# Optimization experiments

Hardware: AMD Instinct MI355X
Metric: run time of the kernel (lower is better)

## Reference

```python
import jax, jax.numpy as jnp
import numpy as np

R = 8
EPS = 1e-08
EPSS = 1e-12


def _diff_x(x, r):
    left = x[:, :, r:2 * r + 1]
    middle = x[:, :, 2 * r + 1:] - x[:, :, :-2 * r - 1]
    right = x[:, :, -1:] - x[:, :, -2 * r - 1:-r - 1]
    return jnp.concatenate([left, middle, right], axis=2)


def _diff_y(x, r):
    left = x[:, :, :, r:2 * r + 1]
    middle = x[:, :, :, 2 * r + 1:] - x[:, :, :, :-2 * r - 1]
    right = x[:, :, :, -1:] - x[:, :, :, -2 * r - 1:-r - 1]
    return jnp.concatenate([left, middle, right], axis=3)


def box_filter(x, r):
    # cumsum-based (2r+1)x(2r+1) box sum with clamped borders (matches torch BoxFilter)
    return _diff_y(jnp.cumsum(_diff_x(jnp.cumsum(x, axis=2), r), axis=3), r)


def bilinear_resize(x, H, W):
    # F.interpolate(mode='bilinear', align_corners=True) for NCHW
    n, c, h, w = x.shape
    ys = jnp.linspace(0.0, h - 1.0, H)
    xs = jnp.linspace(0.0, w - 1.0, W)
    y0 = jnp.floor(ys).astype(jnp.int32)
    x0 = jnp.floor(xs).astype(jnp.int32)
    y1 = jnp.minimum(y0 + 1, h - 1)
    x1 = jnp.minimum(x0 + 1, w - 1)
    wy = (ys - y0).astype(x.dtype)[None, None, :, None]
    wx = (xs - x0).astype(x.dtype)[None, None, None, :]
    rows = jnp.take(x, y0, axis=2) * (1.0 - wy) + jnp.take(x, y1, axis=2) * wy
    return jnp.take(rows, x0, axis=3) * (1.0 - wx) + jnp.take(rows, x1, axis=3) * wx


def setup_inputs() -> dict:
    key = jax.random.key(0)
    k1, k2, k3, k4 = jax.random.split(key, 4)
    return {
        "lr_x": jax.random.normal(k1, (4, 3, 256, 256), dtype=jnp.float32),
        "lr_y": jax.random.normal(k2, (4, 3, 256, 256), dtype=jnp.float32),
        "hr_x": jax.random.normal(k3, (4, 3, 1024, 1024), dtype=jnp.float32),
        "l_a": jax.random.uniform(k4, (4, 3, 256, 256), dtype=jnp.float32),
    }


def reference(lr_x, lr_y, hr_x, l_a):
    n, c, h, w = lr_x.shape
    _, _, hh, wh = hr_x.shape
    dt = lr_x.dtype

    N = box_filter(jnp.ones((1, 1, h, w), dtype=dt), R)  # local window counts

    l_a = jnp.abs(l_a) + EPSS
    l_t = l_a / jnp.sum(l_a)

    mean_a = box_filter(l_a) if False else box_filter(l_a, R) / N
    mean_a2xy = box_filter(l_a * l_a * lr_x * lr_y, R) / N
    mean_tax = box_filter(l_t * l_a * lr_x, R) / N
    mean_ay = box_filter(l_a * lr_y, R) / N
    mean_a2x2 = box_filter(l_a * l_a * lr_x * lr_x, R) / N
    mean_ax = box_filter(l_a * lr_x, R) / N

    temp = jnp.abs(mean_a2x2 - N * mean_tax * mean_ax)
    A = (mean_a2xy - N * mean_tax * mean_ay) / (temp + EPS)
    b = (mean_ay - A * mean_ax) / mean_a

    A = box_filter(A, R) / N
    b = box_filter(b, R) / N

    mean_A = bilinear_resize(A, hh, wh)
    mean_b = bilinear_resize(b, hh, wh)
    return (mean_A * hr_x + mean_b).astype(jnp.float32)
```

## Files before the change

### kernel.cpp

```cpp
#include <hip/hip_runtime.h>

#define RAD 8
#define HH 256
#define WW 256
#define NC 12
#define PS (HH*WW)
#define SCALE (255.0f/1023.0f)

#define NA2 36
#define NC2 20
#define AP2 37
#define HP2 21

__device__ __forceinline__ int swz3072(int b) { return (b & 7) * 384 + (b >> 3); }

__device__ __forceinline__ float run17(float x) {
    float s = x + __shfl_up(x, 1, 64);
    s += __shfl_up(s, 2, 64);
    s += __shfl_up(s, 4, 64);
    s += __shfl_up(s, 8, 64);
    s += __shfl_up(x, 16, 64);
    return s;
}

__global__ __launch_bounds__(256) void k_reduce(const float* __restrict__ la,
                                                float* __restrict__ partials) {
    int tid = threadIdx.x;
    __shared__ float ls[4];
    const float4* p4 = (const float4*)la;
    int base = blockIdx.x * 2048 + tid;
    float s = 0.f;
    #pragma unroll
    for (int i = 0; i < 8; i++) {
        float4 v = p4[base + i * 256];
        s += (fabsf(v.x) + 1e-12f) + (fabsf(v.y) + 1e-12f) +
             (fabsf(v.z) + 1e-12f) + (fabsf(v.w) + 1e-12f);
    }
    for (int off = 32; off > 0; off >>= 1) s += __shfl_down(s, off, 64);
    int lane = tid & 63, wid = tid >> 6;
    if (lane == 0) ls[wid] = s;
    __syncthreads();
    if (tid == 0) partials[blockIdx.x] = ls[0] + ls[1] + ls[2] + ls[3];
}

__global__ __launch_bounds__(256) void k_tile(const float* __restrict__ la,
                                              const float* __restrict__ lx,
                                              const float* __restrict__ ly,
                                              const float* __restrict__ hrx,
                                              const float* __restrict__ partials,
                                              float* __restrict__ out) {
    __shared__ float sA[NA2 * AP2], sB[NA2 * AP2];
    __shared__ float sHA[NA2 * HP2], sHB[NA2 * HP2];
    float* mAb = sA;
    float* mBb = sB;

    int tid = threadIdx.x, lane = tid & 63, wv = tid >> 6;
    int b  = swz3072(blockIdx.x);
    int p  = b >> 8;
    int t  = b & 255;
    int ti = t >> 4, tj = t & 15;
    int I0 = ti << 6, J0 = tj << 6;
    int Lr0 = max(0, (I0 * 255) / 1023 - 1);
    int Lc0 = max(0, (J0 * 255) / 1023 - 1);

    float psum = partials[lane] + ((lane < 32) ? partials[lane + 64] : 0.0f);
    #pragma unroll
    for (int off = 32; off > 0; off >>= 1) psum += __shfl_xor(psum, off, 64);
    float invS = 1.0f / psum;

    {
        int C0  = Lc0 - 8;
        int col = C0 - 8 + lane;
        bool vc = (col >= 0) && (col < WW);
        int colc = min(max(col, 0), WW - 1);
        const float* pa = la + p * PS + colc;
        const float* px = lx + p * PS + colc;
        const float* py = ly + p * PS + colc;

        int  cA    = C0 - 16 + lane;
        int  cIdx  = lane - 16;
        bool vLane = (lane >= 16) && (lane < 16 + NA2);
        bool vcA   = (cA >= 0) && (cA < WW);
        float cxA  = (float)(min(cA + RAD, WW - 1) - max(cA - RAD, 0) + 1);

        float s0 = 0, s1 = 0, s2 = 0, s3 = 0, s4 = 0, s5 = 0;
        auto accum = [&](int rr, float sg) {
            float va = 0.f, vx = 0.f, vy = 0.f;
            if (vc) { int o = rr * WW; va = pa[o]; vx = px[o]; vy = py[o]; }
            float a  = vc ? (fabsf(va) + 1e-12f) : 0.f;
            float ax = a * vx, ay = a * vy;
            s0 = fmaf(sg, a, s0); s1 = fmaf(sg, ax, s1); s2 = fmaf(sg, ay, s2);
            s3 = fmaf(sg, a * ax, s3); s4 = fmaf(sg, ax * ax, s4); s5 = fmaf(sg, ax * ay, s5);
        };

        int R0 = Lr0 - 8 + 9 * wv;
        #pragma unroll
        for (int d = -8; d <= 8; ++d) {
            int rr = R0 + d;
            if (rr >= 0 && rr < HH) accum(rr, 1.0f);
        }
        #pragma unroll
        for (int k = 0; k < 9; ++k) {
            int m = R0 + k;
            if (k > 0) {
                int ra = m + 8; if (ra >= 0 && ra < HH) accum(ra, 1.0f);
                int rs = m - 9; if (rs >= 0 && rs < HH) accum(rs, -1.0f);
            }
            float h0 = run17(s0), h1 = run17(s1), h2 = run17(s2),
                  h3 = run17(s3), h4 = run17(s4), h5 = run17(s5);
            float Av = 0.f, bv = 0.f;
            if (m >= 0 && m < HH) {
                float cy = (float)(min(m + RAD, HH - 1) - max(m - RAD, 0) + 1);
                float Nv = cxA * cy, invN = 1.0f / Nv;
                float m_a = h0 * invN, m_ax = h1 * invN, m_ay = h2 * invN;
                float m_tax = h3 * invN * invS;
                float m_a2x2 = h4 * invN, m_a2xy = h5 * invN;
                float tempv = fabsf(m_a2x2 - Nv * m_tax * m_ax);
                float Avt = (m_a2xy - Nv * m_tax * m_ay) / (tempv + 1e-8f);
                float bvt = (m_ay - Avt * m_ax) / m_a;
                if (vcA) { Av = Avt; bv = bvt; }
            }
            if (vLane) {
                int rIdx = 9 * wv + k;
                sA[rIdx * AP2 + cIdx] = Av;
                sB[rIdx * AP2 + cIdx] = bv;
            }
        }
    }
    __syncthreads();

    for (int job = tid; job < 2 * NA2 * NC2; job += 256) {
        int which = (job >= NA2 * NC2);
        int rest  = which ? job - NA2 * NC2 : job;
        int r = rest / NC2, c = rest - r * NC2;
        const float* rp = (which ? sB : sA) + r * AP2 + c;
        float s = 0.f;
        #pragma unroll
        for (int j = 0; j < 17; ++j) s += rp[j];
        (which ? sHB : sHA)[r * HP2 + c] = s;
    }
    __syncthreads();

    for (int job = tid; job < 2 * NC2 * NC2; job += 256) {
        int which = (job >= NC2 * NC2);
        int rest  = which ? job - NC2 * NC2 : job;
        int r = rest / NC2, c = rest - r * NC2;
        const float* sp = (which ? sHB : sHA) + r * HP2 + c;
        float s = 0.f;
        #pragma unroll
        for (int j = 0; j < 17; ++j) s += sp[j * HP2];
        int gj = Lc0 + c, gi = Lr0 + r;
        float cxw = (float)(min(gj + RAD, WW - 1) - max(gj - RAD, 0) + 1);
        float cyw = (float)(min(gi + RAD, HH - 1) - max(gi - RAD, 0) + 1);
        (which ? mBb : mAb)[r * HP2 + c] = s / (cxw * cyw);
    }
    __syncthreads();

    {
        int col4 = tid & 15;
        int rg   = tid >> 4;
        int J4 = (J0 >> 2) + col4;
        int Jp = J4 << 2;
        int xb = (int)((float)Jp * SCALE);
        int i1 = min(xb + 1, WW - 1), i2 = min(xb + 2, WW - 1);
        int lxb = xb - Lc0, li1 = i1 - Lc0, li2 = i2 - Lc0;
        float wxv[4]; bool hs[4];
        #pragma unroll
        for (int k = 0; k < 4; k++) {
            float xsk = (float)(Jp + k) * SCALE;
            int x0 = (int)xsk;
            wxv[k] = xsk - (float)x0;
            hs[k] = (x0 > xb);
        }
        const float4* h4 = (const float4*)hrx;
        float4* o4 = (float4*)out;
        int planeHR = p * 262144;

        int hidx0 = planeHR + (I0 + 0 * 16 + rg) * 256 + J4;
        int hidx1 = planeHR + (I0 + 1 * 16 + rg) * 256 + J4;
        int hidx2 = planeHR + (I0 + 2 * 16 + rg) * 256 + J4;
        int hidx3 = planeHR + (I0 + 3 * 16 + rg) * 256 + J4;
        float4 hp0 = h4[hidx0], hp1 = h4[hidx1], hp2 = h4[hidx2], hp3 = h4[hidx3];

        #pragma unroll
        for (int it = 0; it < 4; ++it) {
            int row = (it << 4) + rg;
            int I = I0 + row;
            float ysf = (float)I * SCALE;
            int y0 = (int)ysf;
            float wy = ysf - (float)y0;
            int y1 = min(y0 + 1, HH - 1);
            int ly0 = y0 - Lr0, ly1 = y1 - Lr0;
            const float* a0p = mAb + ly0 * HP2;
            const float* a1p = mAb + ly1 * HP2;
            const float* b0p = mBb + ly0 * HP2;
            const float* b1p = mBb + ly1 * HP2;
            float A0a = a0p[lxb], A0b = a0p[li1], A0c = a0p[li2];
            float A1a = a1p[lxb], A1b = a1p[li1], A1c = a1p[li2];
            float B0a = b0p[lxb], B0b = b0p[li1], B0c = b0p[li2];
            float B1a = b1p[lxb], B1b = b1p[li1], B1c = b1p[li2];
            float4 h = (it == 0) ? hp0 : (it == 1) ? hp1 : (it == 2) ? hp2 : hp3;
            int hidx = (it == 0) ? hidx0 : (it == 1) ? hidx1 : (it == 2) ? hidx2 : hidx3;
            float hv[4] = {h.x, h.y, h.z, h.w};
            float ov[4];
            float omwy = 1.0f - wy;
            #pragma unroll
            for (int k = 0; k < 4; k++) {
                bool hb = hs[k];
                float Alo0 = hb ? A0b : A0a, Ahi0 = hb ? A0c : A0b;
                float Alo1 = hb ? A1b : A1a, Ahi1 = hb ? A1c : A1b;
                float Blo0 = hb ? B0b : B0a, Bhi0 = hb ? B0c : B0b;
                float Blo1 = hb ? B1b : B1a, Bhi1 = hb ? B1c : B1b;
                float wx = wxv[k], omwx = 1.0f - wx;
                float Ar0 = Alo0 * omwx + Ahi0 * wx;
                float Ar1 = Alo1 * omwx + Ahi1 * wx;
                float Br0 = Blo0 * omwx + Bhi0 * wx;
                float Br1 = Blo1 * omwx + Bhi1 * wx;
                float Avv = Ar0 * omwy + Ar1 * wy;
                float Bvv = Br0 * omwy + Br1 * wy;
                ov[k] = Avv * hv[k] + Bvv;
            }
            float4 o; o.x = ov[0]; o.y = ov[1]; o.z = ov[2]; o.w = ov[3];
            o4[hidx] = o;
        }
    }
}

extern "C" void kernel_launch(void* const* d_in, const int* in_sizes, int n_in,
                              void* d_out, int out_size, void* d_ws, size_t ws_size,
                              hipStream_t stream) {
    const float* lr_x = (const float*)d_in[0];
    const float* lr_y = (const float*)d_in[1];
    const float* hr_x = (const float*)d_in[2];
    const float* l_a  = (const float*)d_in[3];
    float* out = (float*)d_out;
    float* partials = (float*)d_ws;

    k_reduce<<<96, 256, 0, stream>>>(l_a, partials);
    k_tile  <<<3072, 256, 0, stream>>>(l_a, lr_x, lr_y, hr_x, partials, out);
}
```

Before: 161.4 us.

## Split A/b computation into separate kernel writing horizontal box sums to workspace

Moves the per-pixel A/b computation and the horizontal 17-wide box sum out of the HR tile kernel into a new k_ab kernel. That kernel writes horizontally filtered A and b planes to global workspace, one band of 4 rows by 32 columns per wave. The tile kernel then only loads a 36x20 slab, applies the vertical sum, and upsamples. This removes the redundant recomputation of overlapping low-res halos across the 3072 HR tiles. The cost is an extra kernel launch and a global round trip of two full low-res planes per channel.

```diff
diff --git a/kernel.cpp b/kernel.cpp
--- a/kernel.cpp
+++ b/kernel.cpp
@@ -7,12 +7,12 @@
 #define PS (HH*WW)
 #define SCALE (255.0f/1023.0f)
 
-#define NA2 36
-#define NC2 20
-#define AP2 37
-#define HP2 21
+#define NR3 36
+#define NC3 20
+#define P3  21
 
 __device__ __forceinline__ int swz3072(int b) { return (b & 7) * 384 + (b >> 3); }
+__device__ __forceinline__ int swz1536(int b) { return (b & 7) * 192 + (b >> 3); }
 
 __device__ __forceinline__ float run17(float x) {
     float s = x + __shfl_up(x, 1, 64);
@@ -43,18 +43,91 @@
     if (tid == 0) partials[blockIdx.x] = ls[0] + ls[1] + ls[2] + ls[3];
 }
 
-__global__ __launch_bounds__(256) void k_tile(const float* __restrict__ la,
-                                              const float* __restrict__ lx,
-                                              const float* __restrict__ ly,
+__global__ __launch_bounds__(256) void k_ab(const float* __restrict__ la,
+                                            const float* __restrict__ lx,
+                                            const float* __restrict__ ly,
+                                            const float* __restrict__ partials,
+                                            float* __restrict__ HA,
+                                            float* __restrict__ HB) {
+    int tid = threadIdx.x, lane = tid & 63, wv = tid >> 6;
+    int gw = swz1536(blockIdx.x) * 4 + wv;
+    int p  = gw >> 9;
+    int r  = gw & 511;
+    int strip = r >> 6;
+    int band  = r & 63;
+    int i0 = band << 2;
+    int C0 = strip << 5;
+    int col = C0 - 16 + lane;
+    bool vc = (col >= 0) && (col < WW);
+    int colc = min(max(col, 0), WW - 1);
+    const float* pa = la + p * PS + colc;
+    const float* px = lx + p * PS + colc;
+    const float* py = ly + p * PS + colc;
+
+    float psum = partials[lane] + ((lane < 32) ? partials[lane + 64] : 0.0f);
+    #pragma unroll
+    for (int off = 32; off > 0; off >>= 1) psum += __shfl_xor(psum, off, 64);
+    float invS = 1.0f / psum;
+
+    int  cA  = C0 - 24 + lane;
+    bool vcA = (cA >= 0) && (cA < WW);
+    float cxA = (float)(min(cA + RAD, WW - 1) - max(cA - RAD, 0) + 1);
+    int  cM  = C0 - 32 + lane;
+
+    float s0 = 0, s1 = 0, s2 = 0, s3 = 0, s4 = 0, s5 = 0;
+    auto accum = [&](int rr, float sg) {
+        float va = 0.f, vx = 0.f, vy = 0.f;
+        if (vc) { int o = rr * WW; va = pa[o]; vx = px[o]; vy = py[o]; }
+        float a  = vc ? (fabsf(va) + 1e-12f) : 0.f;
+        float ax = a * vx, ay = a * vy;
+        s0 = fmaf(sg, a, s0); s1 = fmaf(sg, ax, s1); s2 = fmaf(sg, ay, s2);
+        s3 = fmaf(sg, a * ax, s3); s4 = fmaf(sg, ax * ax, s4); s5 = fmaf(sg, ax * ay, s5);
+    };
+
+    #pragma unroll
+    for (int d = -8; d <= 8; ++d) {
+        int rr = i0 + d;
+        if (rr >= 0 && rr < HH) accum(rr, 1.0f);
+    }
+
+    float* HApl = HA + p * PS;
+    float* HBpl = HB + p * PS;
+    #pragma unroll
+    for (int k = 0; k < 4; ++k) {
+        int m = i0 + k;
+        if (k > 0) {
+            int ra = m + 8; if (ra < HH) accum(ra, 1.0f);
+            int rs = m - 9; if (rs >= 0) accum(rs, -1.0f);
+        }
+        float h0 = run17(s0), h1 = run17(s1), h2 = run17(s2),
+              h3 = run17(s3), h4 = run17(s4), h5 = run17(s5);
+        float cy = (float)(min(m + RAD, HH - 1) - max(m - RAD, 0) + 1);
+        float Nv = cxA * cy, invN = 1.0f / Nv;
+        float m_a = h0 * invN, m_ax = h1 * invN, m_ay = h2 * invN;
+        float m_tax = h3 * invN * invS;
+        float m_a2x2 = h4 * invN, m_a2xy = h5 * invN;
+        float tempv = fabsf(m_a2x2 - Nv * m_tax * m_ax);
+        float Avt = (m_a2xy - Nv * m_tax * m_ay) / (tempv + 1e-8f);
+        float bvt = (m_ay - Avt * m_ax) / m_a;
+        float Av = vcA ? Avt : 0.f;
+        float bv = vcA ? bvt : 0.f;
+        float HtA = run17(Av), HtB = run17(bv);
+        if (lane >= 32) {
+            int o = m * WW + cM;
+            HApl[o] = HtA;
+            HBpl[o] = HtB;
+        }
+    }
+}
+
+__global__ __launch_bounds__(256) void k_tile(const float* __restrict__ HA,
+                                              const float* __restrict__ HB,
                                               const float* __restrict__ hrx,
-                                              const float* __restrict__ partials,
                                               float* __restrict__ out) {
-    __shared__ float sA[NA2 * AP2], sB[NA2 * AP2];
-    __shared__ float sHA[NA2 * HP2], sHB[NA2 * HP2];
-    float* mAb = sA;
-    float* mBb = sB;
-
-    int tid = threadIdx.x, lane = tid & 63, wv = tid >> 6;
+    __shared__ float sHA[NR3 * P3], sHB[NR3 * P3];
+    __shared__ float mAb[NC3 * P3], mBb[NC3 * P3];
+
+    int tid = threadIdx.x;
     int b  = swz3072(blockIdx.x);
     int p  = b >> 8;
     int t  = b & 255;
@@ -63,96 +136,33 @@
     int Lr0 = max(0, (I0 * 255) / 1023 - 1);
     int Lc0 = max(0, (J0 * 255) / 1023 - 1);
 
-    float psum = partials[lane] + ((lane < 32) ? partials[lane + 64] : 0.0f);
-    #pragma unroll
-    for (int off = 32; off > 0; off >>= 1) psum += __shfl_xor(psum, off, 64);
-    float invS = 1.0f / psum;
-
-    {
-        int C0  = Lc0 - 8;
-        int col = C0 - 8 + lane;
-        bool vc = (col >= 0) && (col < WW);
-        int colc = min(max(col, 0), WW - 1);
-        const float* pa = la + p * PS + colc;
-        const float* px = lx + p * PS + colc;
-        const float* py = ly + p * PS + colc;
-
-        int  cA    = C0 - 16 + lane;
-        int  cIdx  = lane - 16;
-        bool vLane = (lane >= 16) && (lane < 16 + NA2);
-        bool vcA   = (cA >= 0) && (cA < WW);
-        float cxA  = (float)(min(cA + RAD, WW - 1) - max(cA - RAD, 0) + 1);
-
-        float s0 = 0, s1 = 0, s2 = 0, s3 = 0, s4 = 0, s5 = 0;
-        auto accum = [&](int rr, float sg) {
-            float va = 0.f, vx = 0.f, vy = 0.f;
-            if (vc) { int o = rr * WW; va = pa[o]; vx = px[o]; vy = py[o]; }
-            float a  = vc ? (fabsf(va) + 1e-12f) : 0.f;
-            float ax = a * vx, ay = a * vy;
-            s0 = fmaf(sg, a, s0); s1 = fmaf(sg, ax, s1); s2 = fmaf(sg, ay, s2);
-            s3 = fmaf(sg, a * ax, s3); s4 = fmaf(sg, ax * ax, s4); s5 = fmaf(sg, ax * ay, s5);
-        };
-
-        int R0 = Lr0 - 8 + 9 * wv;
-        #pragma unroll
-        for (int d = -8; d <= 8; ++d) {
-            int rr = R0 + d;
-            if (rr >= 0 && rr < HH) accum(rr, 1.0f);
-        }
-        #pragma unroll
-        for (int k = 0; k < 9; ++k) {
-            int m = R0 + k;
-            if (k > 0) {
-                int ra = m + 8; if (ra >= 0 && ra < HH) accum(ra, 1.0f);
-                int rs = m - 9; if (rs >= 0 && rs < HH) accum(rs, -1.0f);
-            }
-            float h0 = run17(s0), h1 = run17(s1), h2 = run17(s2),
-                  h3 = run17(s3), h4 = run17(s4), h5 = run17(s5);
-            float Av = 0.f, bv = 0.f;
-            if (m >= 0 && m < HH) {
-                float cy = (float)(min(m + RAD, HH - 1) - max(m - RAD, 0) + 1);
-                float Nv = cxA * cy, invN = 1.0f / Nv;
-                float m_a = h0 * invN, m_ax = h1 * invN, m_ay = h2 * invN;
-                float m_tax = h3 * invN * invS;
-                float m_a2x2 = h4 * invN, m_a2xy = h5 * invN;
-                float tempv = fabsf(m_a2x2 - Nv * m_tax * m_ax);
-                float Avt = (m_a2xy - Nv * m_tax * m_ay) / (tempv + 1e-8f);
-                float bvt = (m_ay - Avt * m_ax) / m_a;
-                if (vcA) { Av = Avt; bv = bvt; }
-            }
-            if (vLane) {
-                int rIdx = 9 * wv + k;
-                sA[rIdx * AP2 + cIdx] = Av;
-                sB[rIdx * AP2 + cIdx] = bv;
-            }
-        }
+    const float* HApl = HA + p * PS;
+    const float* HBpl = HB + p * PS;
+    for (int idx = tid; idx < NR3 * NC3; idx += 256) {
+        int r = idx / NC3, c = idx - r * NC3;
+        int gr = Lr0 - 8 + r, gc = Lc0 + c;
+        float av = 0.f, bv = 0.f;
+        if (gr >= 0 && gr < HH && gc < WW) {
+            int o = gr * WW + gc;
+            av = HApl[o]; bv = HBpl[o];
+        }
+        sHA[r * P3 + c] = av;
+        sHB[r * P3 + c] = bv;
     }
     __syncthreads();
 
-    for (int job = tid; job < 2 * NA2 * NC2; job += 256) {
-        int which = (job >= NA2 * NC2);
-        int rest  = which ? job - NA2 * NC2 : job;
-        int r = rest / NC2, c = rest - r * NC2;
-        const float* rp = (which ? sB : sA) + r * AP2 + c;
+    for (int job = tid; job < 2 * NC3 * NC3; job += 256) {
+        int which = (job >= NC3 * NC3);
+        int rest  = which ? job - NC3 * NC3 : job;
+        int r = rest / NC3, c = rest - r * NC3;
+        const float* sp = (which ? sHB : sHA) + r * P3 + c;
         float s = 0.f;
         #pragma unroll
-        for (int j = 0; j < 17; ++j) s += rp[j];
-        (which ? sHB : sHA)[r * HP2 + c] = s;
-    }
-    __syncthreads();
-
-    for (int job = tid; job < 2 * NC2 * NC2; job += 256) {
-        int which = (job >= NC2 * NC2);
-        int rest  = which ? job - NC2 * NC2 : job;
-        int r = rest / NC2, c = rest - r * NC2;
-        const float* sp = (which ? sHB : sHA) + r * HP2 + c;
-        float s = 0.f;
-        #pragma unroll
-        for (int j = 0; j < 17; ++j) s += sp[j * HP2];
+        for (int j = 0; j < 17; ++j) s += sp[j * P3];
         int gj = Lc0 + c, gi = Lr0 + r;
         float cxw = (float)(min(gj + RAD, WW - 1) - max(gj - RAD, 0) + 1);
         float cyw = (float)(min(gi + RAD, HH - 1) - max(gi - RAD, 0) + 1);
-        (which ? mBb : mAb)[r * HP2 + c] = s / (cxw * cyw);
+        (which ? mBb : mAb)[r * P3 + c] = s / (cxw * cyw);
     }
     __syncthreads();
 
@@ -191,10 +201,10 @@
             float wy = ysf - (float)y0;
             int y1 = min(y0 + 1, HH - 1);
             int ly0 = y0 - Lr0, ly1 = y1 - Lr0;
-            const float* a0p = mAb + ly0 * HP2;
-            const float* a1p = mAb + ly1 * HP2;
-            const float* b0p = mBb + ly0 * HP2;
-            const float* b1p = mBb + ly1 * HP2;
+            const float* a0p = mAb + ly0 * P3;
+            const float* a1p = mAb + ly1 * P3;
+            const float* b0p = mBb + ly0 * P3;
+            const float* b1p = mBb + ly1 * P3;
             float A0a = a0p[lxb], A0b = a0p[li1], A0c = a0p[li2];
             float A1a = a1p[lxb], A1b = a1p[li1], A1c = a1p[li2];
             float B0a = b0p[lxb], B0b = b0p[li1], B0c = b0p[li2];
@@ -234,8 +244,13 @@
     const float* hr_x = (const float*)d_in[2];
     const float* l_a  = (const float*)d_in[3];
     float* out = (float*)d_out;
-    float* partials = (float*)d_ws;
+
+    float* ws       = (float*)d_ws;
+    float* partials = ws;
+    float* HA       = ws + 256;
+    float* HB       = HA + NC * PS;
 
     k_reduce<<<96, 256, 0, stream>>>(l_a, partials);
-    k_tile  <<<3072, 256, 0, stream>>>(l_a, lr_x, lr_y, hr_x, partials, out);
-}
+    k_ab    <<<1536, 256, 0, stream>>>(l_a, lr_x, lr_y, partials, HA, HB);
+    k_tile  <<<3072, 256, 0, stream>>>(HA, HB, hr_x, out);
+}
```

After: 136.5 us, median of 2. 15.4% less time.
